# Optimization experiments

Measured on AMD Instinct MI355X. Metric: run time of the kernel, lower is better.

The kernel has to match this reference:

```python
import jax, jax.numpy as jnp
import numpy as np

N, F_IN, H, HEADS, C, E = 4096, 768, 512, 4, 32, 131072
DH = H // HEADS


def gcn_conv(x, W, b, src, dst):
    # PyG GCNConv: add self-loops, symmetric normalization, scatter-add aggregation
    h = x @ W                                   # [N, H_out]
    loop = jnp.arange(N)
    s = jnp.concatenate([src, loop])            # sources incl self-loops
    d = jnp.concatenate([dst, loop])            # targets incl self-loops
    deg = jax.ops.segment_sum(jnp.ones_like(d, dtype=h.dtype), d, num_segments=N)
    dinv = jnp.where(deg > 0, jax.lax.rsqrt(deg), 0.0)
    norm = dinv[s] * dinv[d]                    # [E+N]
    msg = h[s] * norm[:, None]                  # gather + scale
    out = jax.ops.segment_sum(msg, d, num_segments=N)  # scatter-add
    return out + b


def mha(x, in_w, in_b, out_w, out_b):
    # torch.nn.MultiheadAttention, batch=1, q=k=v=x, eval (no dropout)
    qkv = x @ in_w.T + in_b                     # [N, 3H]
    q, k, v = jnp.split(qkv, 3, axis=-1)
    q = q.reshape(N, HEADS, DH)
    k = k.reshape(N, HEADS, DH)
    v = v.reshape(N, HEADS, DH)
    scale = 1.0 / jnp.sqrt(jnp.asarray(DH, x.dtype))
    scores = jnp.einsum('nhd,mhd->hnm', q * scale, k)   # [HEADS, N, N]
    attn = jax.nn.softmax(scores, axis=-1)
    o = jnp.einsum('hnm,mhd->nhd', attn, v).reshape(N, H)
    return o @ out_w.T + out_b


def setup_inputs() -> dict:
    key = jax.random.key(0)
    ks = jax.random.split(key, 12)
    f32 = jnp.float32
    return {
        'x': jax.random.normal(ks[0], (N, F_IN), dtype=f32),
        'edge_index': jax.random.randint(ks[1], (2, E), 0, N, dtype=jnp.int64),
        'W1': jax.random.normal(ks[2], (F_IN, H), dtype=f32) * (1.0 / np.sqrt(F_IN)),
        'b1': jnp.zeros((H,), dtype=f32),
        'in_w': jax.random.normal(ks[3], (3 * H, H), dtype=f32) * (1.0 / np.sqrt(H)),
        'in_b': jnp.zeros((3 * H,), dtype=f32),
        'out_w': jax.random.normal(ks[4], (H, H), dtype=f32) * (1.0 / np.sqrt(H)),
        'out_b': jnp.zeros((H,), dtype=f32),
        'W2': jax.random.normal(ks[5], (H, H), dtype=f32) * (1.0 / np.sqrt(H)),
        'b2': jnp.zeros((H,), dtype=f32),
        'Wc': jax.random.normal(ks[6], (H, C), dtype=f32) * (1.0 / np.sqrt(H)),
        'bc': jnp.zeros((C,), dtype=f32),
    }


def reference(x, edge_index, W1, b1, in_w, in_b, out_w, out_b, W2, b2, Wc, bc):
    src, dst = edge_index[0], edge_index[1]
    h = jax.nn.relu(gcn_conv(x, W1, b1, src, dst))
    h = h + mha(h, in_w, in_b, out_w, out_b)      # residual; dropout is identity (eval)
    h = jax.nn.relu(gcn_conv(h, W2, b2, src, dst))
    return h @ Wc + bc                             # [N, C]
```

## Files before the change

kernel.cpp:

```cpp
#include <hip/hip_runtime.h>

typedef unsigned short u16;
typedef unsigned int u32;
typedef __attribute__((ext_vector_type(8))) short bf16x8;
typedef __attribute__((ext_vector_type(4))) short bf16x4;
typedef __attribute__((ext_vector_type(4))) float f32x4;
typedef __attribute__((ext_vector_type(16))) float f32x16;

__device__ __forceinline__ float b2f(u16 b){ u32 u = ((u32)b)<<16; float f; __builtin_memcpy(&f,&u,4); return f; }
__device__ __forceinline__ u16 f2b(float f){ u32 u; __builtin_memcpy(&u,&f,4); u32 r = (u + 0x7fffu + ((u>>16)&1u)) >> 16; return (u16)r; }
__device__ __forceinline__ u32 cvtpk(float lo, float hi){ u32 r; asm("v_cvt_pk_bf16_f32 %0, %1, %2" : "=v"(r) : "v"(lo), "v"(hi)); return r; }
__device__ __forceinline__ void pswap(u32 &a, u32 &b){ asm("v_permlane32_swap_b32 %0, %1" : "+v"(a), "+v"(b)); }
__device__ __forceinline__ void gload16(const u16* g, u16* l){
  __builtin_amdgcn_global_load_lds((const __attribute__((address_space(1))) void*)g,
                                   (__attribute__((address_space(3))) void*)l, 16, 0, 0);
}

__device__ __forceinline__ void conv_body(const float* __restrict__ in, u16* __restrict__ out, int b, int n){
  int i = (b*256 + threadIdx.x)*4;
  if (i + 3 < n){
    float4 v = *(const float4*)(in + i);
    bf16x4 o;
    o[0]=(short)f2b(v.x); o[1]=(short)f2b(v.y); o[2]=(short)f2b(v.z); o[3]=(short)f2b(v.w);
    *(bf16x4*)(out + i) = o;
  } else {
    for (; i<n; ++i) out[i]=f2b(in[i]);
  }
}
__global__ __launch_bounds__(256) void prep_k(const float* __restrict__ x, const float* __restrict__ inw,
    const float* __restrict__ outw, const float* __restrict__ W1, const float* __restrict__ W2,
    const float* __restrict__ Wc, const int* __restrict__ dst, int E,
    u16* __restrict__ Xb, u16* __restrict__ inWb, u16* __restrict__ outWb,
    u16* __restrict__ W1T, u16* __restrict__ W2T, u16* __restrict__ WcT, int* __restrict__ deg){
  __shared__ float tile[32][33];
  int b = blockIdx.x;
  if (b < 3072){ conv_body(x, Xb, b, 4096*768); return; }
  if (b < 3840){ conv_body(inw, inWb, b-3072, 1536*512); return; }
  if (b < 4096){ conv_body(outw, outWb, b-3840, 512*512); return; }
  if (b < 4752){
    const float* in; u16* out; int R, C, bx, by;
    if (b < 4480){ in=W1; out=W1T; R=768; C=512; int lb=b-4096; bx=lb&15; by=lb>>4; }
    else if (b < 4736){ in=W2; out=W2T; R=512; C=512; int lb=b-4480; bx=lb&15; by=lb>>4; }
    else { in=Wc; out=WcT; R=512; C=32; bx=0; by=b-4736; }
    int tx = threadIdx.x & 31, ty = threadIdx.x >> 5;
    int c0 = bx*32, r0 = by*32;
    #pragma unroll
    for (int k=0;k<4;++k){
      int r = r0 + ty + k*8, c = c0 + tx;
      if (r < R && c < C) tile[ty+k*8][tx] = in[(size_t)r*C + c];
    }
    __syncthreads();
    #pragma unroll
    for (int k=0;k<4;++k){
      int c = c0 + ty + k*8, r = r0 + tx;
      if (r < R && c < C) out[(size_t)c*R + r] = f2b(tile[tx][ty+k*8]);
    }
    return;
  }
  int e = (b-4752)*256 + threadIdx.x;
  if (e < E) atomicAdd(&deg[dst[e]], 1);
}

__global__ __launch_bounds__(256) void scan_k(const int* __restrict__ deg, int* __restrict__ row_ptr,
                                              int* __restrict__ cursor, float* __restrict__ dinv){
  __shared__ int lds[256];
  int t = threadIdx.x;
  int base = t*16;
  int cnt[16]; int s = 0;
  #pragma unroll
  for (int k=0;k<16;++k){
    int d = deg[base+k] + 1;
    cnt[k] = d - 1;
    s += d - 1;
    dinv[base+k] = 1.0f / sqrtf((float)d);
  }
  lds[t] = s; __syncthreads();
  for (int o=1;o<256;o<<=1){
    int v = (t>=o) ? lds[t-o] : 0;
    __syncthreads();
    lds[t] += v;
    __syncthreads();
  }
  int run = lds[t] - s;
  #pragma unroll
  for (int k=0;k<16;++k){ row_ptr[base+k] = run; cursor[base+k] = run; run += cnt[k]; }
  if (t == 255) row_ptr[4096] = run;
}
__global__ __launch_bounds__(256) void scatter_k(const int* __restrict__ src, const int* __restrict__ dst,
                                                 int* __restrict__ cursor, int* __restrict__ srcl, int E){
  int e = blockIdx.x*256 + threadIdx.x;
  if (e < E){
    int d = dst[e];
    int pos = atomicAdd(&cursor[d], 1);
    srcl[pos] = src[e];
  }
}

__global__ __launch_bounds__(128) void aggregate_k(const u16* __restrict__ H, const float* __restrict__ dinv,
                                                   const int* __restrict__ rp, const int* __restrict__ srcl,
                                                   const float* __restrict__ bias, u16* __restrict__ out){
  const int i = blockIdx.x, t = threadIdx.x;
  const float di = dinv[i];
  bf16x4 hv = *(const bf16x4*)(H + (size_t)i*512 + t*4);
  float wself = di*di;
  float a0 = b2f((u16)hv[0])*wself, a1 = b2f((u16)hv[1])*wself, a2 = b2f((u16)hv[2])*wself, a3 = b2f((u16)hv[3])*wself;
  int e0 = rp[i], e1 = rp[i+1];
  int e = e0;
  for (; e+1 < e1; e += 2){
    int s0 = srcl[e], s1 = srcl[e+1];
    float w0 = dinv[s0]*di, w1 = dinv[s1]*di;
    bf16x4 v0 = *(const bf16x4*)(H + (size_t)s0*512 + t*4);
    bf16x4 v1 = *(const bf16x4*)(H + (size_t)s1*512 + t*4);
    a0 += b2f((u16)v0[0])*w0; a1 += b2f((u16)v0[1])*w0; a2 += b2f((u16)v0[2])*w0; a3 += b2f((u16)v0[3])*w0;
    a0 += b2f((u16)v1[0])*w1; a1 += b2f((u16)v1[1])*w1; a2 += b2f((u16)v1[2])*w1; a3 += b2f((u16)v1[3])*w1;
  }
  if (e < e1){
    int s = srcl[e];
    float w = dinv[s]*di;
    bf16x4 v = *(const bf16x4*)(H + (size_t)s*512 + t*4);
    a0 += b2f((u16)v[0])*w; a1 += b2f((u16)v[1])*w; a2 += b2f((u16)v[2])*w; a3 += b2f((u16)v[3])*w;
  }
  a0 += bias[t*4+0]; a1 += bias[t*4+1]; a2 += bias[t*4+2]; a3 += bias[t*4+3];
  a0 = fmaxf(a0,0.f); a1 = fmaxf(a1,0.f); a2 = fmaxf(a2,0.f); a3 = fmaxf(a3,0.f);
  bf16x4 o; o[0]=(short)f2b(a0); o[1]=(short)f2b(a1); o[2]=(short)f2b(a2); o[3]=(short)f2b(a3);
  *(bf16x4*)(out + (size_t)i*512 + t*4) = o;
}

template<int BM,int BN,int WM,int WN,bool BIAS,bool RESID,bool RELU,bool OUTBF,bool QKV>
__global__ __launch_bounds__(256) void gemm_abt_k(
    const u16* __restrict__ A, const u16* __restrict__ B,
    const float* __restrict__ bias, const u16* __restrict__ resid,
    u16* __restrict__ vt, void* __restrict__ Cp, int M, int N, int K)
{
  constexpr int BK = 64;
  constexpr int AISS = (BM*BK)/(256*8);
  constexpr int BISS = (BN*BK)/(256*8);
  constexpr int WC = BN/WN;
  constexpr int FM = WM/16, FN = WN/16;
  constexpr float QS = 0.088388347648318447f * 1.4426950408889634f;
  __shared__ u16 As[BM*BK];
  __shared__ u16 Bs[BN*BK];
  const int tid = threadIdx.x;
  const int wv = tid>>6, ln = tid&63;
  const int l15 = ln&15, l4 = ln>>4;
  const int wm = wv / WC, wn = wv % WC;
  const int bm0 = blockIdx.x*BM, bn0 = blockIdx.y*BN;
  const int arow = tid>>3;
  const int acol = (tid&7)*8;
  f32x4 acc[FM][FN];
  #pragma unroll
  for (int a=0;a<FM;++a)
    #pragma unroll
    for (int b=0;b<FN;++b) acc[a][b] = f32x4{0.f,0.f,0.f,0.f};
  for (int kt=0; kt<K; kt+=BK){
    #pragma unroll
    for (int i=0;i<AISS;++i) gload16(A + (size_t)(bm0 + i*32 + arow)*K + kt + acol, &As[i*2048 + wv*512]);
    #pragma unroll
    for (int i=0;i<BISS;++i) gload16(B + (size_t)(bn0 + i*32 + arow)*K + kt + acol, &Bs[i*2048 + wv*512]);
    __syncthreads();
    #pragma unroll
    for (int kc=0;kc<2;++kc){
      bf16x8 af[FM], bfr[FN];
      #pragma unroll
      for (int a=0;a<FM;++a) af[a] = *(const bf16x8*)(&As[(wm*WM + a*16 + l15)*BK + kc*32 + l4*8]);
      #pragma unroll
      for (int b=0;b<FN;++b) bfr[b] = *(const bf16x8*)(&Bs[(wn*WN + b*16 + l15)*BK + kc*32 + l4*8]);
      #pragma unroll
      for (int a=0;a<FM;++a)
        #pragma unroll
        for (int b=0;b<FN;++b)
          acc[a][b] = __builtin_amdgcn_mfma_f32_16x16x32_bf16(af[a], bfr[b], acc[a][b], 0,0,0);
    }
    __syncthreads();
  }
  #pragma unroll
  for (int a=0;a<FM;++a)
    #pragma unroll
    for (int b=0;b<FN;++b){
      int r0 = bm0 + wm*WM + a*16 + l4*4;
      int c  = bn0 + wn*WN + b*16 + l15;
      if constexpr (QKV){
        float v0 = acc[a][b][0] + bias[c];
        float v1 = acc[a][b][1] + bias[c];
        float v2 = acc[a][b][2] + bias[c];
        float v3 = acc[a][b][3] + bias[c];
        if (c >= 1024){
          bf16x4 pk; pk[0]=(short)f2b(v0); pk[1]=(short)f2b(v1); pk[2]=(short)f2b(v2); pk[3]=(short)f2b(v3);
          *(bf16x4*)(vt + (size_t)(c-1024)*4096 + r0) = pk;
        } else {
          float s = (c < 512) ? QS : 1.0f;
          u16* o = (u16*)Cp;
          o[(size_t)(r0+0)*N + c] = f2b(v0*s);
          o[(size_t)(r0+1)*N + c] = f2b(v1*s);
          o[(size_t)(r0+2)*N + c] = f2b(v2*s);
          o[(size_t)(r0+3)*N + c] = f2b(v3*s);
        }
      } else {
        #pragma unroll
        for (int j=0;j<4;++j){
          int r = r0 + j;
          float v = acc[a][b][j];
          if (BIAS)  v += bias[c];
          if (RESID) v += b2f(resid[(size_t)r*N + c]);
          if (RELU)  v = fmaxf(v, 0.f);
          if (OUTBF) ((u16*)Cp)[(size_t)r*N + c] = f2b(v);
          else       ((float*)Cp)[(size_t)r*N + c] = v;
        }
      }
    }
}

__global__ __launch_bounds__(256) void attn_k(const u16* __restrict__ qkv, const u16* __restrict__ vtg,
                                              u16* __restrict__ Op, float* __restrict__ Lp){
  __shared__ u16 Ks[64*128];
  __shared__ u16 Vs[128*128];
  const int head = blockIdx.y, split = blockIdx.z;
  const int qb0 = blockIdx.x*128;
  const int tid = threadIdx.x, wv = tid>>6, ln = tid&63;
  const int l31 = ln&31, hi = ln>>5;
  bf16x8 qf[8];
  {
    const u16* qp = qkv + (size_t)(qb0 + wv*32 + l31)*1536 + head*128 + hi*8;
    #pragma unroll
    for (int kk=0;kk<8;++kk) qf[kk] = *(const bf16x8*)(qp + kk*16);
  }
  f32x16 acc_o[4];
  #pragma unroll
  for (int d=0;d<4;++d)
    #pragma unroll
    for (int r=0;r<16;++r) acc_o[d][r] = 0.f;
  float l_part = 0.f;
  const int kR = ln, kG = wv*4;
  const int vR = tid>>1, vG = (tid&1)*4;
  const u16* kbase = qkv + 512 + (size_t)head*128;
  const u16* vbase = vtg + (size_t)(head*128 + vR)*4096;
  const int kv00 = split*1024;
  bf16x8 kreg[4], vreg[4];
  #pragma unroll
  for (int i=0;i<4;++i){
    kreg[i] = *(const bf16x8*)(kbase + (size_t)(kv00 + kR)*1536 + (kG+i)*8);
    vreg[i] = *(const bf16x8*)(vbase + kv00 + (vG+i)*8);
  }
  for (int it=0; it<16; ++it){
    #pragma unroll
    for (int i=0;i<4;++i){
      *(bf16x8*)((char*)Ks + kR*256 + (((kG+i)*16) ^ ((kR&15)<<4))) = kreg[i];
      *(bf16x8*)((char*)Vs + vR*256 + (((vG+i)*16) ^ ((vR&15)<<4))) = vreg[i];
    }
    __syncthreads();
    if (it < 15){
      int nb = kv00 + (it+1)*64;
      #pragma unroll
      for (int i=0;i<4;++i){
        kreg[i] = *(const bf16x8*)(kbase + (size_t)(nb + kR)*1536 + (kG+i)*8);
        vreg[i] = *(const bf16x8*)(vbase + nb + (vG+i)*8);
      }
    }
    f32x16 s0, s1;
    #pragma unroll
    for (int r=0;r<16;++r){ s0[r]=0.f; s1[r]=0.f; }
    #pragma unroll
    for (int kk=0;kk<8;++kk){
      int r0 = l31, r1 = 32 + l31;
      bf16x8 k0 = *(const bf16x8*)((char*)Ks + r0*256 + ((kk*32 + hi*16) ^ ((r0&15)<<4)));
      bf16x8 k1 = *(const bf16x8*)((char*)Ks + r1*256 + ((kk*32 + hi*16) ^ ((r1&15)<<4)));
      s0 = __builtin_amdgcn_mfma_f32_32x32x16_bf16(k0, qf[kk], s0, 0,0,0);
      s1 = __builtin_amdgcn_mfma_f32_32x32x16_bf16(k1, qf[kk], s1, 0,0,0);
    }
    union PU { u32 w[4]; bf16x8 v; };
    PU pa[4];
    #pragma unroll
    for (int g=0; g<2; ++g){
      float p[16];
      #pragma unroll
      for (int r=0;r<16;++r){ float sv = g ? s1[r] : s0[r]; p[r] = __builtin_amdgcn_exp2f(sv); l_part += p[r]; }
      u32 c0=cvtpk(p[0],p[1]), c1=cvtpk(p[2],p[3]), c2=cvtpk(p[4],p[5]), c3=cvtpk(p[6],p[7]);
      u32 c4=cvtpk(p[8],p[9]), c5=cvtpk(p[10],p[11]), c6=cvtpk(p[12],p[13]), c7=cvtpk(p[14],p[15]);
      pswap(c0,c2); pswap(c1,c3); pswap(c4,c6); pswap(c5,c7);
      pa[g*2+0].w[0]=c0; pa[g*2+0].w[1]=c1; pa[g*2+0].w[2]=c2; pa[g*2+0].w[3]=c3;
      pa[g*2+1].w[0]=c4; pa[g*2+1].w[1]=c5; pa[g*2+1].w[2]=c6; pa[g*2+1].w[3]=c7;
    }
    #pragma unroll
    for (int dg=0;dg<4;++dg){
      int row = dg*32 + l31;
      #pragma unroll
      for (int kvf=0;kvf<4;++kvf){
        bf16x8 vf = *(const bf16x8*)((char*)Vs + row*256 + ((kvf*32 + hi*16) ^ ((row&15)<<4)));
        acc_o[dg] = __builtin_amdgcn_mfma_f32_32x32x16_bf16(pa[kvf].v, vf, acc_o[dg], 0,0,0);
      }
    }
    __syncthreads();
  }
  float l_tot = l_part + __shfl_xor(l_part, 32, 64);
  if (hi == 0) Lp[split*4096 + qb0 + wv*32 + l31] = l_tot;
  #pragma unroll
  for (int dg=0;dg<4;++dg){
    #pragma unroll
    for (int r=0;r<16;++r){
      int q = qb0 + wv*32 + (r&3) + ((r>>2)<<3) + hi*4;
      Op[((size_t)split*4096 + q)*512 + head*128 + dg*32 + l31] = f2b(acc_o[dg][r]);
    }
  }
}

__global__ __launch_bounds__(256) void combine_k(const u16* __restrict__ Op, const float* __restrict__ Lp,
                                                 u16* __restrict__ oatt){
  int idx = blockIdx.x*256 + threadIdx.x;
  int n = idx >> 6, c8 = (idx & 63) << 3;
  float l = 0.f;
  #pragma unroll
  for (int s=0;s<4;++s) l += Lp[s*4096+n];
  float inv = 1.0f/l;
  float acc[8] = {0,0,0,0,0,0,0,0};
  #pragma unroll
  for (int s=0;s<4;++s){
    bf16x8 v = *(const bf16x8*)(Op + ((size_t)(s*4096+n))*512 + c8);
    #pragma unroll
    for (int j=0;j<8;++j) acc[j] += b2f((u16)v[j]);
  }
  bf16x8 o;
  #pragma unroll
  for (int j=0;j<8;++j) o[j] = (short)f2b(acc[j]*inv);
  *(bf16x8*)(oatt + (size_t)n*512 + c8) = o;
}

extern "C" void kernel_launch(void* const* d_in, const int* in_sizes, int n_in,
                              void* d_out, int out_size, void* d_ws, size_t ws_size,
                              hipStream_t stream) {
  (void)n_in; (void)out_size; (void)ws_size;
  const float* x    = (const float*)d_in[0];
  const int*   ei   = (const int*)d_in[1];
  const float* W1   = (const float*)d_in[2];
  const float* b1   = (const float*)d_in[3];
  const float* inw  = (const float*)d_in[4];
  const float* inb  = (const float*)d_in[5];
  const float* outw = (const float*)d_in[6];
  const float* outb = (const float*)d_in[7];
  const float* W2   = (const float*)d_in[8];
  const float* b2   = (const float*)d_in[9];
  const float* Wc   = (const float*)d_in[10];
  const float* bc   = (const float*)d_in[11];
  float* out = (float*)d_out;
  const int E = in_sizes[1] / 2;
  const int* srcp = ei;
  const int* dstp = ei + E;

  char* base = (char*)d_ws;
  size_t off = 0;
  auto alloc = [&](size_t bytes)->void*{
    void* p = base + off;
    off = (off + bytes + 255) & ~((size_t)255);
    return p;
  };
  u16* Xb    = (u16*)alloc((size_t)4096*768*2);
  u16* W1T   = (u16*)alloc((size_t)512*768*2);
  u16* inWb  = (u16*)alloc((size_t)1536*512*2);
  u16* outWb = (u16*)alloc((size_t)512*512*2);
  u16* W2T   = (u16*)alloc((size_t)512*512*2);
  u16* WcT   = (u16*)alloc((size_t)32*512*2);
  u16* Hpre  = (u16*)alloc((size_t)4096*512*2);
  u16* h1    = (u16*)alloc((size_t)4096*512*2);
  u16* qkvb  = (u16*)alloc((size_t)4096*1536*2);
  u16* vtg   = (u16*)alloc((size_t)512*4096*2);
  u16* oatt  = (u16*)alloc((size_t)4096*512*2);
  u16* h2    = (u16*)alloc((size_t)4096*512*2);
  u16* h3    = (u16*)alloc((size_t)4096*512*2);
  u16* Opart = (u16*)alloc((size_t)4*4096*512*2);
  float* Lpart = (float*)alloc((size_t)4*4096*4);
  int*   deg  = (int*)alloc(4096*4);
  float* dinv = (float*)alloc(4096*4);
  int*   rowp = (int*)alloc(4097*4);
  int*   curs = (int*)alloc(4096*4);
  int*   srcl = (int*)alloc((size_t)E*4);

  hipMemsetAsync(deg, 0, 4096*sizeof(int), stream);
  int degBlocks = (E + 255)/256;
  prep_k<<<4752 + degBlocks, 256, 0, stream>>>(x, inw, outw, W1, W2, Wc, dstp, E,
                                               Xb, inWb, outWb, W1T, W2T, WcT, deg);
  scan_k<<<1,256,0,stream>>>(deg, rowp, curs, dinv);
  scatter_k<<<(E+255)/256,256,0,stream>>>(srcp, dstp, curs, srcl, E);

  gemm_abt_k<128,64,64,32,false,false,false,true,false><<<dim3(32,8),256,0,stream>>>(Xb, W1T, nullptr, nullptr, nullptr, Hpre, 4096, 512, 768);
  aggregate_k<<<4096,128,0,stream>>>(Hpre, dinv, rowp, srcl, b1, h1);

  gemm_abt_k<128,64,64,32,true,false,false,true,true><<<dim3(32,24),256,0,stream>>>(h1, inWb, inb, nullptr, vtg, qkvb, 4096, 1536, 512);
  attn_k<<<dim3(32,4,4),256,0,stream>>>(qkvb, vtg, Opart, Lpart);
  combine_k<<<1024,256,0,stream>>>(Opart, Lpart, oatt);
  gemm_abt_k<128,64,64,32,true,true,false,true,false><<<dim3(32,8),256,0,stream>>>(oatt, outWb, outb, h1, nullptr, h2, 4096, 512, 512);

  gemm_abt_k<128,64,64,32,false,false,false,true,false><<<dim3(32,8),256,0,stream>>>(h2, W2T, nullptr, nullptr, nullptr, Hpre, 4096, 512, 512);
  aggregate_k<<<4096,128,0,stream>>>(Hpre, dinv, rowp, srcl, b2, h3);

  gemm_abt_k<64,32,16,32,true,false,false,false,false><<<dim3(64,1),256,0,stream>>>(h3, WcT, bc, nullptr, nullptr, out, 4096, 32, 512);
}
```

Baseline: 182.3 us.

## Read attention K/V fragments directly from global memory and unroll aggregation by four

The attention kernel no longer stages K and V tiles through shared memory with a register prefetch and block barriers. Each wave now loads its MFMA K and V fragments straight from global memory, relying on L1/L2 to serve the reuse across the four waves in a block. This removes LDS traffic and __syncthreads, but it quadruples global/cache load requests and exposes load latency without explicit prefetch. The GCN aggregation loop is also unrolled from two to four neighbors to raise memory-level parallelism.

```diff
diff --git a/kernel.cpp b/kernel.cpp
--- a/kernel.cpp
+++ b/kernel.cpp
@@ -106,15 +106,19 @@
   float a0 = b2f((u16)hv[0])*wself, a1 = b2f((u16)hv[1])*wself, a2 = b2f((u16)hv[2])*wself, a3 = b2f((u16)hv[3])*wself;
   int e0 = rp[i], e1 = rp[i+1];
   int e = e0;
-  for (; e+1 < e1; e += 2){
-    int s0 = srcl[e], s1 = srcl[e+1];
-    float w0 = dinv[s0]*di, w1 = dinv[s1]*di;
+  for (; e+3 < e1; e += 4){
+    int s0 = srcl[e], s1 = srcl[e+1], s2 = srcl[e+2], s3 = srcl[e+3];
+    float w0 = dinv[s0]*di, w1 = dinv[s1]*di, w2 = dinv[s2]*di, w3 = dinv[s3]*di;
     bf16x4 v0 = *(const bf16x4*)(H + (size_t)s0*512 + t*4);
     bf16x4 v1 = *(const bf16x4*)(H + (size_t)s1*512 + t*4);
+    bf16x4 v2 = *(const bf16x4*)(H + (size_t)s2*512 + t*4);
+    bf16x4 v3 = *(const bf16x4*)(H + (size_t)s3*512 + t*4);
     a0 += b2f((u16)v0[0])*w0; a1 += b2f((u16)v0[1])*w0; a2 += b2f((u16)v0[2])*w0; a3 += b2f((u16)v0[3])*w0;
     a0 += b2f((u16)v1[0])*w1; a1 += b2f((u16)v1[1])*w1; a2 += b2f((u16)v1[2])*w1; a3 += b2f((u16)v1[3])*w1;
-  }
-  if (e < e1){
+    a0 += b2f((u16)v2[0])*w2; a1 += b2f((u16)v2[1])*w2; a2 += b2f((u16)v2[2])*w2; a3 += b2f((u16)v2[3])*w2;
+    a0 += b2f((u16)v3[0])*w3; a1 += b2f((u16)v3[1])*w3; a2 += b2f((u16)v3[2])*w3; a3 += b2f((u16)v3[3])*w3;
+  }
+  for (; e < e1; ++e){
     int s = srcl[e];
     float w = dinv[s]*di;
     bf16x4 v = *(const bf16x4*)(H + (size_t)s*512 + t*4);
@@ -212,15 +216,13 @@
 
 __global__ __launch_bounds__(256) void attn_k(const u16* __restrict__ qkv, const u16* __restrict__ vtg,
                                               u16* __restrict__ Op, float* __restrict__ Lp){
-  __shared__ u16 Ks[64*128];
-  __shared__ u16 Vs[128*128];
   const int head = blockIdx.y, split = blockIdx.z;
-  const int qb0 = blockIdx.x*128;
   const int tid = threadIdx.x, wv = tid>>6, ln = tid&63;
+  const int qb0 = blockIdx.x*128 + wv*32;
   const int l31 = ln&31, hi = ln>>5;
   bf16x8 qf[8];
   {
-    const u16* qp = qkv + (size_t)(qb0 + wv*32 + l31)*1536 + head*128 + hi*8;
+    const u16* qp = qkv + (size_t)(qb0 + l31)*1536 + head*128 + hi*8;
     #pragma unroll
     for (int kk=0;kk<8;++kk) qf[kk] = *(const bf16x8*)(qp + kk*16);
   }
@@ -230,40 +232,18 @@
     #pragma unroll
     for (int r=0;r<16;++r) acc_o[d][r] = 0.f;
   float l_part = 0.f;
-  const int kR = ln, kG = wv*4;
-  const int vR = tid>>1, vG = (tid&1)*4;
-  const u16* kbase = qkv + 512 + (size_t)head*128;
-  const u16* vbase = vtg + (size_t)(head*128 + vR)*4096;
+  const u16* kb = qkv + 512 + (size_t)head*128;
+  const u16* vb = vtg + (size_t)head*128*4096;
   const int kv00 = split*1024;
-  bf16x8 kreg[4], vreg[4];
-  #pragma unroll
-  for (int i=0;i<4;++i){
-    kreg[i] = *(const bf16x8*)(kbase + (size_t)(kv00 + kR)*1536 + (kG+i)*8);
-    vreg[i] = *(const bf16x8*)(vbase + kv00 + (vG+i)*8);
-  }
   for (int it=0; it<16; ++it){
-    #pragma unroll
-    for (int i=0;i<4;++i){
-      *(bf16x8*)((char*)Ks + kR*256 + (((kG+i)*16) ^ ((kR&15)<<4))) = kreg[i];
-      *(bf16x8*)((char*)Vs + vR*256 + (((vG+i)*16) ^ ((vR&15)<<4))) = vreg[i];
-    }
-    __syncthreads();
-    if (it < 15){
-      int nb = kv00 + (it+1)*64;
-      #pragma unroll
-      for (int i=0;i<4;++i){
-        kreg[i] = *(const bf16x8*)(kbase + (size_t)(nb + kR)*1536 + (kG+i)*8);
-        vreg[i] = *(const bf16x8*)(vbase + nb + (vG+i)*8);
-      }
-    }
+    const int kvb = kv00 + it*64;
     f32x16 s0, s1;
     #pragma unroll
     for (int r=0;r<16;++r){ s0[r]=0.f; s1[r]=0.f; }
     #pragma unroll
     for (int kk=0;kk<8;++kk){
-      int r0 = l31, r1 = 32 + l31;
-      bf16x8 k0 = *(const bf16x8*)((char*)Ks + r0*256 + ((kk*32 + hi*16) ^ ((r0&15)<<4)));
-      bf16x8 k1 = *(const bf16x8*)((char*)Ks + r1*256 + ((kk*32 + hi*16) ^ ((r1&15)<<4)));
+      bf16x8 k0 = *(const bf16x8*)(kb + (size_t)(kvb + l31)*1536 + kk*16 + hi*8);
+      bf16x8 k1 = *(const bf16x8*)(kb + (size_t)(kvb + 32 + l31)*1536 + kk*16 + hi*8);
       s0 = __builtin_amdgcn_mfma_f32_32x32x16_bf16(k0, qf[kk], s0, 0,0,0);
       s1 = __builtin_amdgcn_mfma_f32_32x32x16_bf16(k1, qf[kk], s1, 0,0,0);
     }
@@ -282,22 +262,21 @@
     }
     #pragma unroll
     for (int dg=0;dg<4;++dg){
-      int row = dg*32 + l31;
+      const u16* vr = vb + (size_t)(dg*32 + l31)*4096 + kvb;
       #pragma unroll
       for (int kvf=0;kvf<4;++kvf){
-        bf16x8 vf = *(const bf16x8*)((char*)Vs + row*256 + ((kvf*32 + hi*16) ^ ((row&15)<<4)));
+        bf16x8 vf = *(const bf16x8*)(vr + kvf*16 + hi*8);
         acc_o[dg] = __builtin_amdgcn_mfma_f32_32x32x16_bf16(pa[kvf].v, vf, acc_o[dg], 0,0,0);
       }
     }
-    __syncthreads();
   }
   float l_tot = l_part + __shfl_xor(l_part, 32, 64);
-  if (hi == 0) Lp[split*4096 + qb0 + wv*32 + l31] = l_tot;
+  if (hi == 0) Lp[split*4096 + qb0 + l31] = l_tot;
   #pragma unroll
   for (int dg=0;dg<4;++dg){
     #pragma unroll
     for (int r=0;r<16;++r){
-      int q = qb0 + wv*32 + (r&3) + ((r>>2)<<3) + hi*4;
+      int q = qb0 + (r&3) + ((r>>2)<<3) + hi*4;
       Op[((size_t)split*4096 + q)*512 + head*128 + dg*32 + l31] = f2b(acc_o[dg][r]);
     }
   }
```

Result: slower. 263.9 us (+44.8%).
